# Kernel optimization log

Hardware: AMD Instinct MI355X
Metric: run time of the kernel (lower is better)

Reference implementation:

```python
import jax, jax.numpy as jnp
import numpy as np

B, N, C = 8, 2048, 3
E, H, NB, K = 256, 8, 3, 32
OUT_PTS = N // 2
EPS = 1e-5


def _ln(x, g, b):
    mu = jnp.mean(x, -1, keepdims=True)
    v = jnp.var(x, -1, keepdims=True)
    return g * (x - mu) / jnp.sqrt(v + EPS) + b


def _bn(x, g, b, axes):
    # train-mode BatchNorm1d: per-feature batch stats (biased variance)
    mu = jnp.mean(x, axes, keepdims=True)
    v = jnp.var(x, axes, keepdims=True)
    return g * (x - mu) / jnp.sqrt(v + EPS) + b


def setup_inputs() -> dict:
    key = jax.random.key(0)
    ks = jax.random.split(key, 20)
    rn = lambda k, shape, s: jax.random.normal(k, shape, jnp.float32) * s
    inp = {}
    inp['x'] = jax.random.normal(ks[0], (B, N, C), jnp.float32)
    # ARPE params
    inp['W1'] = rn(ks[1], (2 * C, 2 * C), 0.3)
    inp['b1'] = jnp.zeros((2 * C,), jnp.float32)
    inp['g1'] = jnp.ones((2 * C,), jnp.float32)
    inp['be1'] = jnp.zeros((2 * C,), jnp.float32)
    inp['W2'] = rn(ks[2], (2 * C, E), 0.3)
    inp['b2'] = jnp.zeros((E,), jnp.float32)
    inp['g2'] = jnp.ones((E,), jnp.float32)
    inp['be2'] = jnp.zeros((E,), jnp.float32)
    # transformer block params (stacked over NB blocks)
    inp['ln1_g'] = jnp.ones((NB, E), jnp.float32)
    inp['ln1_b'] = jnp.zeros((NB, E), jnp.float32)
    inp['attn_w'] = rn(ks[3], (NB, E, 3 * E), 0.02)
    inp['attn_b'] = jnp.zeros((NB, 3 * E), jnp.float32)
    inp['out_w'] = rn(ks[4], (NB, E, E), 0.02)
    inp['out_b'] = jnp.zeros((NB, E), jnp.float32)
    inp['ln2_g'] = jnp.ones((NB, E), jnp.float32)
    inp['ln2_b'] = jnp.zeros((NB, E), jnp.float32)
    inp['ff1_w'] = rn(ks[5], (NB, E, 2 * E), 0.02)
    inp['ff1_b'] = jnp.zeros((NB, 2 * E), jnp.float32)
    inp['ff2_w'] = rn(ks[6], (NB, 2 * E, E), 0.02)
    inp['ff2_b'] = jnp.zeros((NB, E), jnp.float32)
    # decoder params
    inp['dec1_w'] = rn(ks[7], (E, 2 * E), 0.02)
    inp['dec1_b'] = jnp.zeros((2 * E,), jnp.float32)
    inp['dec2_w'] = rn(ks[8], (2 * E, OUT_PTS * 3), 0.02)
    inp['dec2_b'] = jnp.zeros((OUT_PTS * 3,), jnp.float32)
    return inp


def _forward(x, W1, b1, g1, be1, W2, b2, g2, be2,
             ln1_g, ln1_b, attn_w, attn_b, out_w, out_b,
             ln2_g, ln2_b, ff1_w, ff1_b, ff2_w, ff2_b,
             dec1_w, dec1_b, dec2_w, dec2_b):
    Bv, Nv, Cv = x.shape
    # --- ARPE: KNN gather + diff-concat + MLP/BN/ELU + max-pool ---
    sq = jnp.sum(x * x, -1)  # [B,N]
    d2 = sq[:, :, None] + sq[:, None, :] - 2.0 * jnp.einsum('bnc,bmc->bnm', x, x)
    idx = jax.lax.top_k(-d2, K)[1]  # [B,N,K] nearest (incl. self)
    knn = jax.vmap(lambda pts, i: pts[i])(x, idx)  # [B,N,K,C]
    diffs = x[:, :, None, :] - knn
    feat = jnp.concatenate([jnp.broadcast_to(x[:, :, None, :], diffs.shape), diffs], -1)  # [B,N,K,2C]
    h = feat @ W1 + b1
    h = jax.nn.elu(_bn(h, g1, be1, (0, 1, 2)))
    h = jnp.max(h, axis=2)  # max-pool over K -> [B,N,2C]
    h = h @ W2 + b2
    h = jax.nn.elu(_bn(h, g2, be2, (0, 1)))  # [B,N,E]
    # --- transformer blocks (pre-LN; residual adds the LN'd x, per source) ---
    dh = E // H
    scale = 1.0 / np.sqrt(dh)
    xcur = h
    for i in range(NB):
        hn = _ln(xcur, ln1_g[i], ln1_b[i])
        qkv = hn @ attn_w[i] + attn_b[i]
        q, k_, v = jnp.split(qkv, 3, axis=-1)
        q = q.reshape(Bv, Nv, H, dh)
        k_ = k_.reshape(Bv, Nv, H, dh)
        v = v.reshape(Bv, Nv, H, dh)
        att = jax.nn.softmax(jnp.einsum('bnhd,bmhd->bhnm', q, k_) * scale, axis=-1)
        o = jnp.einsum('bhnm,bmhd->bnhd', att, v).reshape(Bv, Nv, E)
        xcur = o @ out_w[i] + out_b[i] + hn
        hn2 = _ln(xcur, ln2_g[i], ln2_b[i])
        ff = jax.nn.gelu(hn2 @ ff1_w[i] + ff1_b[i], approximate=False) @ ff2_w[i] + ff2_b[i]
        xcur = ff + xcur
    # --- decoder ---
    m = jnp.mean(xcur, axis=1)  # [B,E]
    d = jax.nn.gelu(m @ dec1_w + dec1_b, approximate=False) @ dec2_w + dec2_b
    return d.reshape(Bv, OUT_PTS, 3)


def reference(x, W1, b1, g1, be1, W2, b2, g2, be2,
              ln1_g, ln1_b, attn_w, attn_b, out_w, out_b,
              ln2_g, ln2_b, ff1_w, ff1_b, ff2_w, ff2_b,
              dec1_w, dec1_b, dec2_w, dec2_b):
    return _forward(x, W1, b1, g1, be1, W2, b2, g2, be2,
                    ln1_g, ln1_b, attn_w, attn_b, out_w, out_b,
                    ln2_g, ln2_b, ff1_w, ff1_b, ff2_w, ff2_b,
                    dec1_w, dec1_b, dec2_w, dec2_b)
```

## Files before the change

kernel.cpp:

```cpp
#include <hip/hip_runtime.h>
#include <math.h>
#include <float.h>

#define Bb 8
#define Nn 2048
#define Ee 256
#define Hh 8
#define NB 3
#define KK 32
#define DH 32
#define QKV 768
#define FF 512
#define OUTPTS 1024

#define CEXP 0.25509667991878083f

typedef __bf16 bf16x8 __attribute__((ext_vector_type(8)));
typedef __bf16 bf16x4 __attribute__((ext_vector_type(4)));
typedef float f32x4 __attribute__((ext_vector_type(4)));
typedef float f32x16 __attribute__((ext_vector_type(16)));
typedef unsigned u32x2 __attribute__((ext_vector_type(2)));

#if __has_builtin(__builtin_amdgcn_exp2f)
#define EXP2(x) __builtin_amdgcn_exp2f(x)
#else
#define EXP2(x) exp2f(x)
#endif

static __device__ __forceinline__ float geluf(float v) {
    return 0.5f * v * (1.0f + erff(v * 0.70710678118654752f));
}
static __device__ __forceinline__ float eluf(float v) {
    return v > 0.0f ? v : expm1f(v);
}
static __device__ __forceinline__ unsigned pkbf(float a, float b) {
    union { __bf16 h[2]; unsigned u; } t;
    t.h[0] = (__bf16)a; t.h[1] = (__bf16)b;
    return t.u;
}
static __device__ __forceinline__ void swap32(unsigned a, unsigned b, unsigned& outA, unsigned& outB, int hi) {
#if __has_builtin(__builtin_amdgcn_permlane32_swap)
    u32x2 r = __builtin_amdgcn_permlane32_swap(a, b, false, false);
    outA = r[0]; outB = r[1];
#else
    unsigned ax = (unsigned)__shfl_xor((int)a, 32, 64);
    unsigned bx = (unsigned)__shfl_xor((int)b, 32, 64);
    outB = hi ? ax : b;
    outA = hi ? a : bx;
#endif
}

#if __has_builtin(__builtin_amdgcn_global_load_lds)
#define HAVE_GLOAD_LDS 1
static __device__ __forceinline__ void gl_lds16(const __bf16* g, __bf16* l) {
    __builtin_amdgcn_global_load_lds(
        (const __attribute__((address_space(1))) unsigned*)g,
        (__attribute__((address_space(3))) unsigned*)l, 16, 0, 0);
}
#else
#define HAVE_GLOAD_LDS 0
#endif

__global__ __launch_bounds__(256) void k_knn(const float* __restrict__ x,
                                             int* __restrict__ idx) {
    int q = blockIdx.x * 4 + (threadIdx.x >> 6);
    int lane = threadIdx.x & 63;
    int b = q >> 11, n = q & (Nn - 1);
    const float* xb = x + (size_t)b * Nn * 3;
    float xn0 = xb[n * 3], xn1 = xb[n * 3 + 1], xn2 = xb[n * 3 + 2];
    float sqn = xn0 * xn0 + xn1 * xn1 + xn2 * xn2;

    unsigned cand[32];
#pragma unroll
    for (int c = 0; c < 32; ++c) {
        int m = lane + 64 * c;
        float xm0 = xb[m * 3], xm1 = xb[m * 3 + 1], xm2 = xb[m * 3 + 2];
        float sqm = xm0 * xm0 + xm1 * xm1 + xm2 * xm2;
        float d = sqn + sqm - 2.0f * (xn0 * xm0 + xn1 * xm1 + xn2 * xm2);
        unsigned fb = __float_as_uint(d);
        cand[c] = (fb & 0x80000000u) ? ~fb : (fb | 0x80000000u);
    }

    unsigned prefix = 0u;
    for (int bit = 31; bit >= 0; --bit) {
        unsigned t = prefix | (1u << bit);
        int cnt = 0;
#pragma unroll
        for (int c = 0; c < 32; ++c)
            cnt += (int)__popcll(__ballot(cand[c] < t));
        if (cnt < KK) prefix = t;
    }

    unsigned long long lmask = (1ULL << lane) - 1ULL;
    int base = 0;
#pragma unroll
    for (int c = 0; c < 32; ++c) {
        bool sel = cand[c] < prefix;
        unsigned long long mk = __ballot(sel);
        int pos = base + (int)__popcll(mk & lmask);
        if (sel) idx[(size_t)q * KK + pos] = lane + 64 * c;
        base += (int)__popcll(mk);
    }
    for (int c = 0; c < 32 && base < KK; ++c) {
        bool eq = (cand[c] == prefix);
        unsigned long long mk = __ballot(eq);
        int pos = base + (int)__popcll(mk & lmask);
        if (eq && pos < KK) idx[(size_t)q * KK + pos] = lane + 64 * c;
        base += (int)__popcll(mk);
    }
}

__global__ __launch_bounds__(256) void k_h1(const float* __restrict__ x, const int* __restrict__ idx,
                                            const float* __restrict__ W1, const float* __restrict__ b1,
                                            float* __restrict__ h1) {
    int t = blockIdx.x * 256 + threadIdx.x;
    if (t >= Bb * Nn * KK) return;
    int bn = t / KK;
    int b = bn / Nn, n = bn % Nn;
    int j = idx[t];
    const float* xb = x + (size_t)b * Nn * 3;
    float xn0 = xb[n * 3], xn1 = xb[n * 3 + 1], xn2 = xb[n * 3 + 2];
    float f3 = xn0 - xb[j * 3], f4 = xn1 - xb[j * 3 + 1], f5 = xn2 - xb[j * 3 + 2];
    float* o = h1 + (size_t)t * 6;
#pragma unroll
    for (int c = 0; c < 6; ++c) {
        o[c] = b1[c] + xn0 * W1[0 * 6 + c] + xn1 * W1[1 * 6 + c] + xn2 * W1[2 * 6 + c]
             + f3 * W1[3 * 6 + c] + f4 * W1[4 * 6 + c] + f5 * W1[5 * 6 + c];
    }
}

__global__ __launch_bounds__(256) void k_stats6_part(const float* __restrict__ v, int R, int nblk,
                                                     double* __restrict__ part) {
    int blk = blockIdx.x, tid = threadIdx.x;
    int rows = R / nblk;
    int r0 = blk * rows;
    double s[6] = {0, 0, 0, 0, 0, 0}, s2[6] = {0, 0, 0, 0, 0, 0};
    for (int r = r0 + tid; r < r0 + rows; r += 256) {
        const float* p = v + (size_t)r * 6;
#pragma unroll
        for (int c = 0; c < 6; ++c) { double t = p[c]; s[c] += t; s2[c] += t * t; }
    }
    __shared__ double sh[256][12];
#pragma unroll
    for (int c = 0; c < 6; ++c) { sh[tid][c] = s[c]; sh[tid][6 + c] = s2[c]; }
    __syncthreads();
    for (int st = 128; st > 0; st >>= 1) {
        if (tid < st) {
#pragma unroll
            for (int q = 0; q < 12; ++q) sh[tid][q] += sh[tid + st][q];
        }
        __syncthreads();
    }
    if (tid < 12) part[(size_t)blk * 12 + tid] = sh[0][tid];
}

__global__ __launch_bounds__(64) void k_stats6_fin(const double* __restrict__ part, int nblk, int R,
                                                   float* __restrict__ mean, float* __restrict__ rstd) {
    int q = threadIdx.x;
    __shared__ double tot[12];
    if (q < 12) {
        double s = 0.0;
        for (int b = 0; b < nblk; ++b) s += part[(size_t)b * 12 + q];
        tot[q] = s;
    }
    __syncthreads();
    if (q < 6) {
        double mu = tot[q] / R;
        double var = tot[6 + q] / R - mu * mu;
        mean[q] = (float)mu;
        rstd[q] = (float)(1.0 / sqrt(var + 1e-5));
    }
}

__global__ __launch_bounds__(256) void k_stats256_part(const float* __restrict__ v, int R, int nblk,
                                                       double* __restrict__ part) {
    int blk = blockIdx.x, c = threadIdx.x;
    int rows = R / nblk;
    int r0 = blk * rows;
    double s = 0.0, s2 = 0.0;
    for (int r = r0; r < r0 + rows; ++r) {
        double t = v[(size_t)r * Ee + c];
        s += t; s2 += t * t;
    }
    part[(size_t)blk * (2 * Ee) + c] = s;
    part[(size_t)blk * (2 * Ee) + Ee + c] = s2;
}

__global__ __launch_bounds__(256) void k_stats256_fin(const double* __restrict__ part, int nblk, int R,
                                                      float* __restrict__ mean, float* __restrict__ rstd) {
    int c = threadIdx.x;
    double s = 0.0, s2 = 0.0;
    for (int b = 0; b < nblk; ++b) {
        s += part[(size_t)b * (2 * Ee) + c];
        s2 += part[(size_t)b * (2 * Ee) + Ee + c];
    }
    double mu = s / R;
    double var = s2 / R - mu * mu;
    mean[c] = (float)mu;
    rstd[c] = (float)(1.0 / sqrt(var + 1e-5));
}

__global__ __launch_bounds__(256) void k_maxh2(const float* __restrict__ h1,
                                               const float* __restrict__ mean1, const float* __restrict__ rstd1,
                                               const float* __restrict__ g1, const float* __restrict__ be1,
                                               const float* __restrict__ W2, const float* __restrict__ b2,
                                               float* __restrict__ x0) {
    int bn = blockIdx.x;
    int t = threadIdx.x;
    __shared__ float hval[KK][6];
    __shared__ float hmax[6];
    if (t < KK * 6) {
        int k = t / 6, c = t % 6;
        float v = h1[((size_t)bn * KK + k) * 6 + c];
        v = (v - mean1[c]) * rstd1[c] * g1[c] + be1[c];
        hval[k][c] = eluf(v);
    }
    __syncthreads();
    if (t < 6) {
        float m = -FLT_MAX;
        for (int k = 0; k < KK; ++k) m = fmaxf(m, hval[k][t]);
        hmax[t] = m;
    }
    __syncthreads();
    float s = b2[t];
#pragma unroll
    for (int i = 0; i < 6; ++i) s += hmax[i] * W2[i * Ee + t];
    x0[(size_t)bn * Ee + t] = s;
}

__global__ __launch_bounds__(256) void k_bn2apply(float* __restrict__ x0,
                                                  const float* __restrict__ mean2, const float* __restrict__ rstd2,
                                                  const float* __restrict__ g2, const float* __restrict__ be2) {
    int i = blockIdx.x * 256 + threadIdx.x;
    if (i < Bb * Nn * Ee) {
        int c = i & (Ee - 1);
        float v = (x0[i] - mean2[c]) * rstd2[c] * g2[c] + be2[c];
        x0[i] = eluf(v);
    }
}

__global__ __launch_bounds__(256) void k_lnb(const float* __restrict__ X,
                                             const float* __restrict__ g, const float* __restrict__ b,
                                             __bf16* __restrict__ Yb) {
    int row = blockIdx.x * 4 + (threadIdx.x >> 6);
    int lane = threadIdx.x & 63;
    float4 v = *(const float4*)(X + (size_t)row * Ee + lane * 4);
    float s = v.x + v.y + v.z + v.w;
#pragma unroll
    for (int off = 32; off; off >>= 1) s += __shfl_xor(s, off, 64);
    float mu = s * (1.0f / Ee);
    float d0 = v.x - mu, d1 = v.y - mu, d2 = v.z - mu, d3 = v.w - mu;
    float s2 = d0 * d0 + d1 * d1 + d2 * d2 + d3 * d3;
#pragma unroll
    for (int off = 32; off; off >>= 1) s2 += __shfl_xor(s2, off, 64);
    float rstd = 1.0f / sqrtf(s2 * (1.0f / Ee) + 1e-5f);
    float4 gv = *(const float4*)(g + lane * 4);
    float4 bv = *(const float4*)(b + lane * 4);
    bf16x4 o;
    o[0] = (__bf16)(gv.x * d0 * rstd + bv.x);
    o[1] = (__bf16)(gv.y * d1 * rstd + bv.y);
    o[2] = (__bf16)(gv.z * d2 * rstd + bv.z);
    o[3] = (__bf16)(gv.w * d3 * rstd + bv.w);
    *(bf16x4*)(Yb + (size_t)row * Ee + lane * 4) = o;
}

__global__ __launch_bounds__(256) void k_wt(const float* __restrict__ w, __bf16* __restrict__ wt,
                                            int K, int N) {
    w += (size_t)blockIdx.z * K * N;
    wt += (size_t)blockIdx.z * K * N;
    int n0 = blockIdx.x * 64, k0 = blockIdx.y * 64;
    __shared__ float L[64][65];
    int t = threadIdx.x;
    int r = t >> 4, c4 = (t & 15) * 4;
#pragma unroll
    for (int j = 0; j < 4; ++j) {
        float4 v = *(const float4*)(w + (size_t)(k0 + r + j * 16) * N + n0 + c4);
        L[r + j * 16][c4 + 0] = v.x; L[r + j * 16][c4 + 1] = v.y;
        L[r + j * 16][c4 + 2] = v.z; L[r + j * 16][c4 + 3] = v.w;
    }
    __syncthreads();
#pragma unroll
    for (int j = 0; j < 4; ++j) {
        int nn = r + j * 16;
        bf16x4 o;
        o[0] = (__bf16)L[c4 + 0][nn]; o[1] = (__bf16)L[c4 + 1][nn];
        o[2] = (__bf16)L[c4 + 2][nn]; o[3] = (__bf16)L[c4 + 3][nn];
        *(bf16x4*)(wt + (size_t)(n0 + nn) * K + k0 + c4) = o;
    }
}

template<int OUTM, int RESM, int ACT, int QKVM>
__global__ __launch_bounds__(256) void k_mgemm(const __bf16* __restrict__ Ain,
                                               const __bf16* __restrict__ Wt,
                                               const float* __restrict__ bias,
                                               const void* __restrict__ res,
                                               void* __restrict__ out,
                                               int Kd, int Nd) {
    __shared__ __bf16 As[128 * 32];
    __shared__ __bf16 Bs[128 * 32];
    int tid = threadIdx.x;
    int n0 = blockIdx.x * 128, m0 = blockIdx.y * 128;
    int wave = tid >> 6, lane = tid & 63;
    int wr = wave >> 1, wc = wave & 1;
    int t = lane & 15, gg = lane >> 4;
    f32x4 acc[4][4];
#pragma unroll
    for (int m = 0; m < 4; ++m)
#pragma unroll
        for (int nn = 0; nn < 4; ++nn) acc[m][nn] = (f32x4){0.f, 0.f, 0.f, 0.f};
    int r0 = tid >> 2, g0 = tid & 3;
    int r1 = (tid + 256) >> 2, g1 = tid & 3;
    for (int kt = 0; kt < Kd; kt += 32) {
#if HAVE_GLOAD_LDS
        __syncthreads();
        gl_lds16(Ain + (size_t)(m0 + r0) * Kd + kt + g0 * 8, &As[r0 * 32 + g0 * 8]);
        gl_lds16(Ain + (size_t)(m0 + r1) * Kd + kt + g1 * 8, &As[r1 * 32 + g1 * 8]);
        gl_lds16(Wt + (size_t)(n0 + r0) * Kd + kt + g0 * 8, &Bs[r0 * 32 + g0 * 8]);
        gl_lds16(Wt + (size_t)(n0 + r1) * Kd + kt + g1 * 8, &Bs[r1 * 32 + g1 * 8]);
        __syncthreads();
#else
        bf16x8 a0 = *(const bf16x8*)(Ain + (size_t)(m0 + r0) * Kd + kt + g0 * 8);
        bf16x8 a1 = *(const bf16x8*)(Ain + (size_t)(m0 + r1) * Kd + kt + g1 * 8);
        bf16x8 w0 = *(const bf16x8*)(Wt + (size_t)(n0 + r0) * Kd + kt + g0 * 8);
        bf16x8 w1 = *(const bf16x8*)(Wt + (size_t)(n0 + r1) * Kd + kt + g1 * 8);
        __syncthreads();
        *(bf16x8*)&As[r0 * 32 + g0 * 8] = a0;
        *(bf16x8*)&As[r1 * 32 + g1 * 8] = a1;
        *(bf16x8*)&Bs[r0 * 32 + g0 * 8] = w0;
        *(bf16x8*)&Bs[r1 * 32 + g1 * 8] = w1;
        __syncthreads();
#endif
        bf16x8 af[4], bfr[4];
#pragma unroll
        for (int m = 0; m < 4; ++m) af[m] = *(const bf16x8*)&As[(wr * 64 + m * 16 + t) * 32 + gg * 8];
#pragma unroll
        for (int nn = 0; nn < 4; ++nn) bfr[nn] = *(const bf16x8*)&Bs[(wc * 64 + nn * 16 + t) * 32 + gg * 8];
#pragma unroll
        for (int m = 0; m < 4; ++m)
#pragma unroll
            for (int nn = 0; nn < 4; ++nn)
                acc[m][nn] = __builtin_amdgcn_mfma_f32_16x16x32_bf16(af[m], bfr[nn], acc[m][nn], 0, 0, 0);
    }
#pragma unroll
    for (int m = 0; m < 4; ++m) {
#pragma unroll
        for (int nn = 0; nn < 4; ++nn) {
            int ocol = n0 + wc * 64 + nn * 16 + t;
            float bv = bias[ocol];
#pragma unroll
            for (int j = 0; j < 4; ++j) {
                int orow = m0 + wr * 64 + m * 16 + gg * 4 + j;
                float v = acc[m][nn][j] + bv;
                if (RESM == 1) v += (float)((const __bf16*)res)[(size_t)orow * Nd + ocol];
                if (RESM == 2) v += ((const float*)res)[(size_t)orow * Nd + ocol];
                if (ACT == 1) v = geluf(v);
                if (QKVM == 1 && ocol < Ee) v *= CEXP;
                if (OUTM == 0) ((float*)out)[(size_t)orow * Nd + ocol] = v;
                else           ((__bf16*)out)[(size_t)orow * Nd + ocol] = (__bf16)v;
            }
        }
    }
}

__global__ __launch_bounds__(256) void k_attn(const __bf16* __restrict__ qkv, __bf16* __restrict__ obf) {
    int wgid = (blockIdx.x & 7) * 128 + (blockIdx.x >> 3);
    int qg = wgid & 15;
    int bh = wgid >> 4;
    int h = bh & 7, b = bh >> 3;
    int wave = threadIdx.x >> 6, lane = threadIdx.x & 63;
    int l31 = lane & 31, hi = lane >> 5;
    int qb = qg * 128 + wave * 32;
    const size_t base = (size_t)b * Nn * QKV;

    const __bf16* qrow = qkv + base + (size_t)(qb + l31) * QKV + h * DH;
    bf16x8 qf0 = *(const bf16x8*)(qrow + hi * 8);
    bf16x8 qf1 = *(const bf16x8*)(qrow + 16 + hi * 8);

    const __bf16* vbase = qkv + base + 2 * Ee + h * DH + l31;

    f32x16 oacc = {0.f,0.f,0.f,0.f,0.f,0.f,0.f,0.f,0.f,0.f,0.f,0.f,0.f,0.f,0.f,0.f};
    float lsum = 0.0f;

    for (int c0 = 0; c0 < Nn; c0 += 32) {
        const __bf16* krow = qkv + base + (size_t)(c0 + l31) * QKV + Ee + h * DH;
        bf16x8 kf0 = *(const bf16x8*)(krow + hi * 8);
        bf16x8 kf1 = *(const bf16x8*)(krow + 16 + hi * 8);

        f32x16 s = {0.f,0.f,0.f,0.f,0.f,0.f,0.f,0.f,0.f,0.f,0.f,0.f,0.f,0.f,0.f,0.f};
        s = __builtin_amdgcn_mfma_f32_32x32x16_bf16(kf0, qf0, s, 0, 0, 0);
        s = __builtin_amdgcn_mfma_f32_32x32x16_bf16(kf1, qf1, s, 0, 0, 0);

        float p[16];
#pragma unroll
        for (int i = 0; i < 16; ++i) p[i] = EXP2(s[i]);
        float s0 = (p[0] + p[1]) + (p[2] + p[3]);
        float s1 = (p[4] + p[5]) + (p[6] + p[7]);
        float s2r = (p[8] + p[9]) + (p[10] + p[11]);
        float s3 = (p[12] + p[13]) + (p[14] + p[15]);
        lsum += (s0 + s1) + (s2r + s3);

        unsigned d0 = pkbf(p[0], p[1]),  d1 = pkbf(p[2], p[3]);
        unsigned d2 = pkbf(p[4], p[5]),  d3 = pkbf(p[6], p[7]);
        unsigned d4 = pkbf(p[8], p[9]),  d5 = pkbf(p[10], p[11]);
        unsigned d6 = pkbf(p[12], p[13]), d7 = pkbf(p[14], p[15]);
        unsigned w0a, w0b, w1a, w1b, w2a, w2b, w3a, w3b;
        swap32(d2, d0, w2a, w0a, hi);
        swap32(d3, d1, w3a, w1a, hi);
        swap32(d6, d4, w2b, w0b, hi);
        swap32(d7, d5, w3b, w1b, hi);
        union { unsigned u[4]; bf16x8 v; } pa0, pa1;
        pa0.u[0] = w0a; pa0.u[1] = w1a; pa0.u[2] = w2a; pa0.u[3] = w3a;
        pa1.u[0] = w0b; pa1.u[1] = w1b; pa1.u[2] = w2b; pa1.u[3] = w3b;

        union { __bf16 hh[8]; bf16x8 v; } vf0, vf1;
        const __bf16* vp = vbase + (size_t)(c0 + hi * 8) * QKV;
#pragma unroll
        for (int j = 0; j < 8; ++j) vf0.hh[j] = vp[(size_t)j * QKV];
#pragma unroll
        for (int j = 0; j < 8; ++j) vf1.hh[j] = vp[(size_t)(16 + j) * QKV];

        oacc = __builtin_amdgcn_mfma_f32_32x32x16_bf16(pa0.v, vf0.v, oacc, 0, 0, 0);
        oacc = __builtin_amdgcn_mfma_f32_32x32x16_bf16(pa1.v, vf1.v, oacc, 0, 0, 0);
    }

    float ltot = lsum + __shfl_xor(lsum, 32, 64);
    float invl = 1.0f / ltot;
#pragma unroll
    for (int reg = 0; reg < 16; ++reg) {
        int row = (reg & 3) + 8 * (reg >> 2) + 4 * hi;
        float iv = __shfl(invl, row, 64);
        obf[((size_t)(b * Nn + qb + row)) * Ee + h * DH + l31] = (__bf16)(oacc[reg] * iv);
    }
}

__global__ __launch_bounds__(256) void k_meanpart(const float* __restrict__ X, float* __restrict__ pm) {
    int chunk = blockIdx.x, b = blockIdx.y;
    int e = threadIdx.x;
    float s = 0.0f;
    for (int n = chunk * 256; n < chunk * 256 + 256; ++n)
        s += X[((size_t)b * Nn + n) * Ee + e];
    pm[(size_t)(b * 8 + chunk) * Ee + e] = s;
}
__global__ __launch_bounds__(256) void k_meanfin(const float* __restrict__ pm, float* __restrict__ m) {
    int i = blockIdx.x * 256 + threadIdx.x;
    int b = i >> 8, e = i & 255;
    float s = 0.0f;
    for (int c = 0; c < 8; ++c) s += pm[(size_t)(b * 8 + c) * Ee + e];
    m[i] = s * (1.0f / Nn);
}
__global__ __launch_bounds__(512) void k_dec1(const float* __restrict__ m, const float* __restrict__ w,
                                              const float* __restrict__ bias, float* __restrict__ t1) {
    int b = blockIdx.x, j = threadIdx.x;
    float s = bias[j];
    for (int i = 0; i < Ee; ++i) s += m[b * Ee + i] * w[i * FF + j];
    t1[b * FF + j] = geluf(s);
}
__global__ __launch_bounds__(256) void k_dec2(const float* __restrict__ t1, const float* __restrict__ w,
                                              const float* __restrict__ bias, float* __restrict__ out) {
    int i = blockIdx.x * 256 + threadIdx.x;
    int b = i / 3072, j = i % 3072;
    float s = bias[j];
    for (int k = 0; k < FF; ++k) s += t1[b * FF + k] * w[k * 3072 + j];
    out[i] = s;
}

extern "C" void kernel_launch(void* const* d_in, const int* in_sizes, int n_in,
                              void* d_out, int out_size, void* d_ws, size_t ws_size,
                              hipStream_t stream) {
    const float* x      = (const float*)d_in[0];
    const float* W1     = (const float*)d_in[1];
    const float* b1     = (const float*)d_in[2];
    const float* g1     = (const float*)d_in[3];
    const float* be1    = (const float*)d_in[4];
    const float* W2     = (const float*)d_in[5];
    const float* b2     = (const float*)d_in[6];
    const float* g2     = (const float*)d_in[7];
    const float* be2    = (const float*)d_in[8];
    const float* ln1_g  = (const float*)d_in[9];
    const float* ln1_b  = (const float*)d_in[10];
    const float* attn_w = (const float*)d_in[11];
    const float* attn_b = (const float*)d_in[12];
    const float* out_w  = (const float*)d_in[13];
    const float* out_b  = (const float*)d_in[14];
    const float* ln2_g  = (const float*)d_in[15];
    const float* ln2_b  = (const float*)d_in[16];
    const float* ff1_w  = (const float*)d_in[17];
    const float* ff1_b  = (const float*)d_in[18];
    const float* ff2_w  = (const float*)d_in[19];
    const float* ff2_b  = (const float*)d_in[20];
    const float* dec1_w = (const float*)d_in[21];
    const float* dec1_b = (const float*)d_in[22];
    const float* dec2_w = (const float*)d_in[23];
    const float* dec2_b = (const float*)d_in[24];
    (void)in_sizes; (void)n_in; (void)out_size; (void)ws_size;

    const size_t MN = (size_t)Bb * Nn * Ee;

    float*  A    = (float*)d_ws;
    __bf16* Ab   = (__bf16*)(A + MN);
    __bf16* qkvb = Ab + MN;
    __bf16* obf  = qkvb + (size_t)Bb * Nn * QKV;
    __bf16* ffb  = obf + MN;
    __bf16* attn_wt = ffb + (size_t)Bb * Nn * FF;
    __bf16* out_wt  = attn_wt + (size_t)NB * QKV * Ee;
    __bf16* ff1_wt  = out_wt + (size_t)NB * Ee * Ee;
    __bf16* ff2_wt  = ff1_wt + (size_t)NB * FF * Ee;
    float*  S       = (float*)(ff2_wt + (size_t)NB * Ee * FF);

    float* mean1 = S,      *rstd1 = S + 16;
    float* mean2 = S + 32, *rstd2 = S + 32 + Ee;
    float* pm    = S + 1024;
    float* mvec  = pm + 64 * Ee;
    float* t1    = mvec + Bb * Ee;
    double* part6   = (double*)(S + 32768);
    double* part256 = part6 + 512 * 12;

    int*   idx = (int*)qkvb;
    float* h1  = (float*)(idx + (size_t)Bb * Nn * KK);

    k_wt<<<dim3(QKV / 64, Ee / 64, NB), 256, 0, stream>>>(attn_w, attn_wt, Ee, QKV);
    k_wt<<<dim3(Ee / 64, Ee / 64, NB), 256, 0, stream>>>(out_w, out_wt, Ee, Ee);
    k_wt<<<dim3(FF / 64, Ee / 64, NB), 256, 0, stream>>>(ff1_w, ff1_wt, Ee, FF);
    k_wt<<<dim3(Ee / 64, FF / 64, NB), 256, 0, stream>>>(ff2_w, ff2_wt, FF, Ee);

    k_knn <<<Bb * Nn / 4, 256, 0, stream>>>(x, idx);
    k_h1  <<<(Bb * Nn * KK) / 256, 256, 0, stream>>>(x, idx, W1, b1, h1);
    k_stats6_part<<<512, 256, 0, stream>>>(h1, Bb * Nn * KK, 512, part6);
    k_stats6_fin<<<1, 64, 0, stream>>>(part6, 512, Bb * Nn * KK, mean1, rstd1);
    k_maxh2<<<Bb * Nn, 256, 0, stream>>>(h1, mean1, rstd1, g1, be1, W2, b2, A);
    k_stats256_part<<<64, 256, 0, stream>>>(A, Bb * Nn, 64, part256);
    k_stats256_fin<<<1, 256, 0, stream>>>(part256, 64, Bb * Nn, mean2, rstd2);
    k_bn2apply<<<(Bb * Nn * Ee) / 256, 256, 0, stream>>>(A, mean2, rstd2, g2, be2);

    const int M = Bb * Nn;
    for (int i = 0; i < NB; ++i) {
        k_lnb<<<M / 4, 256, 0, stream>>>(A, ln1_g + i * Ee, ln1_b + i * Ee, Ab);
        k_mgemm<1, 0, 0, 1><<<dim3(QKV / 128, M / 128), 256, 0, stream>>>(
            Ab, attn_wt + (size_t)i * QKV * Ee, attn_b + i * QKV, nullptr, qkvb, Ee, QKV);
        k_attn<<<Bb * Hh * 16, 256, 0, stream>>>(qkvb, obf);
        k_mgemm<0, 1, 0, 0><<<dim3(Ee / 128, M / 128), 256, 0, stream>>>(
            obf, out_wt + (size_t)i * Ee * Ee, out_b + i * Ee, Ab, A, Ee, Ee);
        k_lnb<<<M / 4, 256, 0, stream>>>(A, ln2_g + i * Ee, ln2_b + i * Ee, Ab);
        k_mgemm<1, 0, 1, 0><<<dim3(FF / 128, M / 128), 256, 0, stream>>>(
            Ab, ff1_wt + (size_t)i * FF * Ee, ff1_b + i * FF, nullptr, ffb, Ee, FF);
        k_mgemm<0, 2, 0, 0><<<dim3(Ee / 128, M / 128), 256, 0, stream>>>(
            ffb, ff2_wt + (size_t)i * Ee * FF, ff2_b + i * Ee, A, A, FF, Ee);
    }

    k_meanpart<<<dim3(8, Bb), 256, 0, stream>>>(A, pm);
    k_meanfin<<<Bb, 256, 0, stream>>>(pm, mvec);
    k_dec1<<<Bb, FF, 0, stream>>>(mvec, dec1_w, dec1_b, t1);
    k_dec2<<<(Bb * OUTPTS * 3) / 256, 256, 0, stream>>>(t1, dec2_w, dec2_b, (float*)d_out);
}
```

Baseline: 887.1 us.

## Software-pipeline K/V loads in attention and merge weight-transpose launches

The attention inner loop now processes two 32-key chunks per iteration. The next chunk's K and V fragments are prefetched into registers while the current chunk runs its MFMAs, and two separate output accumulators shorten the MFMA dependency chain. This is meant to hide global load latency in the attention kernel, at the cost of more registers and possibly lower occupancy. Separately, the four weight-transpose launches are folded into one kernel that dispatches on block index, removing three launches.

```diff
diff --git a/kernel.cpp b/kernel.cpp
--- a/kernel.cpp
+++ b/kernel.cpp
@@ -264,11 +264,29 @@
     *(bf16x4*)(Yb + (size_t)row * Ee + lane * 4) = o;
 }
 
-__global__ __launch_bounds__(256) void k_wt(const float* __restrict__ w, __bf16* __restrict__ wt,
-                                            int K, int N) {
-    w += (size_t)blockIdx.z * K * N;
-    wt += (size_t)blockIdx.z * K * N;
-    int n0 = blockIdx.x * 64, k0 = blockIdx.y * 64;
+__global__ __launch_bounds__(256) void k_wtall(const float* __restrict__ attn_w, const float* __restrict__ out_w,
+                                               const float* __restrict__ ff1_w, const float* __restrict__ ff2_w,
+                                               __bf16* __restrict__ attn_wt, __bf16* __restrict__ out_wt,
+                                               __bf16* __restrict__ ff1_wt, __bf16* __restrict__ ff2_wt) {
+    int bid = blockIdx.x;
+    const float* w; __bf16* wt; int K, N, n0, k0;
+    if (bid < 144) {
+        int r = bid; int z = r / 48; r %= 48;
+        K = Ee; N = QKV; n0 = (r % 12) * 64; k0 = (r / 12) * 64;
+        w = attn_w + (size_t)z * K * N; wt = attn_wt + (size_t)z * K * N;
+    } else if (bid < 192) {
+        int r = bid - 144; int z = r / 16; r %= 16;
+        K = Ee; N = Ee; n0 = (r % 4) * 64; k0 = (r / 4) * 64;
+        w = out_w + (size_t)z * K * N; wt = out_wt + (size_t)z * K * N;
+    } else if (bid < 288) {
+        int r = bid - 192; int z = r / 32; r %= 32;
+        K = Ee; N = FF; n0 = (r % 8) * 64; k0 = (r / 8) * 64;
+        w = ff1_w + (size_t)z * K * N; wt = ff1_wt + (size_t)z * K * N;
+    } else {
+        int r = bid - 288; int z = r / 32; r %= 32;
+        K = FF; N = Ee; n0 = (r % 4) * 64; k0 = (r / 4) * 64;
+        w = ff2_w + (size_t)z * K * N; wt = ff2_wt + (size_t)z * K * N;
+    }
     __shared__ float L[64][65];
     int t = threadIdx.x;
     int r = t >> 4, c4 = (t & 15) * 4;
@@ -376,20 +394,31 @@
     bf16x8 qf0 = *(const bf16x8*)(qrow + hi * 8);
     bf16x8 qf1 = *(const bf16x8*)(qrow + 16 + hi * 8);
 
+    const __bf16* kbase = qkv + base + Ee + h * DH + (size_t)l31 * QKV;
     const __bf16* vbase = qkv + base + 2 * Ee + h * DH + l31;
 
-    f32x16 oacc = {0.f,0.f,0.f,0.f,0.f,0.f,0.f,0.f,0.f,0.f,0.f,0.f,0.f,0.f,0.f,0.f};
+    f32x16 oaccA = {0.f,0.f,0.f,0.f,0.f,0.f,0.f,0.f,0.f,0.f,0.f,0.f,0.f,0.f,0.f,0.f};
+    f32x16 oaccB = oaccA;
     float lsum = 0.0f;
 
-    for (int c0 = 0; c0 < Nn; c0 += 32) {
-        const __bf16* krow = qkv + base + (size_t)(c0 + l31) * QKV + Ee + h * DH;
-        bf16x8 kf0 = *(const bf16x8*)(krow + hi * 8);
-        bf16x8 kf1 = *(const bf16x8*)(krow + 16 + hi * 8);
-
+    auto loadK = [&](int c, bf16x8& k0, bf16x8& k1) {
+        const __bf16* kr = kbase + (size_t)c * QKV;
+        k0 = *(const bf16x8*)(kr + hi * 8);
+        k1 = *(const bf16x8*)(kr + 16 + hi * 8);
+    };
+    auto loadV = [&](int c, bf16x8& v0, bf16x8& v1) {
+        union { __bf16 hh[8]; bf16x8 v; } a, bb;
+        const __bf16* vp = vbase + (size_t)(c + hi * 8) * QKV;
+#pragma unroll
+        for (int j = 0; j < 8; ++j) a.hh[j] = vp[(size_t)j * QKV];
+#pragma unroll
+        for (int j = 0; j < 8; ++j) bb.hh[j] = vp[(size_t)(16 + j) * QKV];
+        v0 = a.v; v1 = bb.v;
+    };
+    auto compute = [&](bf16x8 k0, bf16x8 k1, bf16x8 v0, bf16x8 v1, f32x16& oacc) {
         f32x16 s = {0.f,0.f,0.f,0.f,0.f,0.f,0.f,0.f,0.f,0.f,0.f,0.f,0.f,0.f,0.f,0.f};
-        s = __builtin_amdgcn_mfma_f32_32x32x16_bf16(kf0, qf0, s, 0, 0, 0);
-        s = __builtin_amdgcn_mfma_f32_32x32x16_bf16(kf1, qf1, s, 0, 0, 0);
-
+        s = __builtin_amdgcn_mfma_f32_32x32x16_bf16(k0, qf0, s, 0, 0, 0);
+        s = __builtin_amdgcn_mfma_f32_32x32x16_bf16(k1, qf1, s, 0, 0, 0);
         float p[16];
 #pragma unroll
         for (int i = 0; i < 16; ++i) p[i] = EXP2(s[i]);
@@ -412,16 +441,21 @@
         pa0.u[0] = w0a; pa0.u[1] = w1a; pa0.u[2] = w2a; pa0.u[3] = w3a;
         pa1.u[0] = w0b; pa1.u[1] = w1b; pa1.u[2] = w2b; pa1.u[3] = w3b;
 
-        union { __bf16 hh[8]; bf16x8 v; } vf0, vf1;
-        const __bf16* vp = vbase + (size_t)(c0 + hi * 8) * QKV;
-#pragma unroll
-        for (int j = 0; j < 8; ++j) vf0.hh[j] = vp[(size_t)j * QKV];
-#pragma unroll
-        for (int j = 0; j < 8; ++j) vf1.hh[j] = vp[(size_t)(16 + j) * QKV];
-
-        oacc = __builtin_amdgcn_mfma_f32_32x32x16_bf16(pa0.v, vf0.v, oacc, 0, 0, 0);
-        oacc = __builtin_amdgcn_mfma_f32_32x32x16_bf16(pa1.v, vf1.v, oacc, 0, 0, 0);
-    }
+        oacc = __builtin_amdgcn_mfma_f32_32x32x16_bf16(pa0.v, v0, oacc, 0, 0, 0);
+        oacc = __builtin_amdgcn_mfma_f32_32x32x16_bf16(pa1.v, v1, oacc, 0, 0, 0);
+    };
+
+    bf16x8 k0a, k1a, v0a, v1a, k0b, k1b, v0b, v1b;
+    loadK(0, k0a, k1a); loadV(0, v0a, v1a);
+    for (int c0 = 0; c0 < Nn; c0 += 64) {
+        loadK(c0 + 32, k0b, k1b); loadV(c0 + 32, v0b, v1b);
+        compute(k0a, k1a, v0a, v1a, oaccA);
+        if (c0 + 64 < Nn) {
+            loadK(c0 + 64, k0a, k1a); loadV(c0 + 64, v0a, v1a);
+        }
+        compute(k0b, k1b, v0b, v1b, oaccB);
+    }
+    f32x16 oacc = oaccA + oaccB;
 
     float ltot = lsum + __shfl_xor(lsum, 32, 64);
     float invl = 1.0f / ltot;
@@ -518,10 +552,8 @@
     int*   idx = (int*)qkvb;
     float* h1  = (float*)(idx + (size_t)Bb * Nn * KK);
 
-    k_wt<<<dim3(QKV / 64, Ee / 64, NB), 256, 0, stream>>>(attn_w, attn_wt, Ee, QKV);
-    k_wt<<<dim3(Ee / 64, Ee / 64, NB), 256, 0, stream>>>(out_w, out_wt, Ee, Ee);
-    k_wt<<<dim3(FF / 64, Ee / 64, NB), 256, 0, stream>>>(ff1_w, ff1_wt, Ee, FF);
-    k_wt<<<dim3(Ee / 64, FF / 64, NB), 256, 0, stream>>>(ff2_w, ff2_wt, FF, Ee);
+    k_wtall<<<384, 256, 0, stream>>>(attn_w, out_w, ff1_w, ff2_w,
+                                     attn_wt, out_wt, ff1_wt, ff2_wt);
 
     k_knn <<<Bb * Nn / 4, 256, 0, stream>>>(x, idx);
     k_h1  <<<(Bb * Nn * KK) / 256, 256, 0, stream>>>(x, idx, W1, b1, h1);
```

After: 951.1 us. 1.07x slower.

## Split attention over key halves with merge kernel; fuse weight transposes

Applied to the files above, without the earlier changes.

Attention now splits the key range in two, doubling the grid, and writes unnormalized partial outputs and row sums. A new merge kernel adds the two partials and divides by the combined sum. The four weight-transpose launches are merged into one kernel that dispatches on block index. This adds extra global traffic for the partial outputs and one more launch per block, in exchange for more parallelism in attention.

```diff
diff --git a/kernel.cpp b/kernel.cpp
--- a/kernel.cpp
+++ b/kernel.cpp
@@ -264,11 +264,29 @@
     *(bf16x4*)(Yb + (size_t)row * Ee + lane * 4) = o;
 }
 
-__global__ __launch_bounds__(256) void k_wt(const float* __restrict__ w, __bf16* __restrict__ wt,
-                                            int K, int N) {
-    w += (size_t)blockIdx.z * K * N;
-    wt += (size_t)blockIdx.z * K * N;
-    int n0 = blockIdx.x * 64, k0 = blockIdx.y * 64;
+__global__ __launch_bounds__(256) void k_wtall(const float* __restrict__ attn_w, const float* __restrict__ out_w,
+                                               const float* __restrict__ ff1_w, const float* __restrict__ ff2_w,
+                                               __bf16* __restrict__ attn_wt, __bf16* __restrict__ out_wt,
+                                               __bf16* __restrict__ ff1_wt, __bf16* __restrict__ ff2_wt) {
+    int bid = blockIdx.x;
+    const float* w; __bf16* wt; int K, N, n0, k0;
+    if (bid < 144) {
+        int r = bid; int z = r / 48; r %= 48;
+        K = Ee; N = QKV; n0 = (r % 12) * 64; k0 = (r / 12) * 64;
+        w = attn_w + (size_t)z * K * N; wt = attn_wt + (size_t)z * K * N;
+    } else if (bid < 192) {
+        int r = bid - 144; int z = r / 16; r %= 16;
+        K = Ee; N = Ee; n0 = (r % 4) * 64; k0 = (r / 4) * 64;
+        w = out_w + (size_t)z * K * N; wt = out_wt + (size_t)z * K * N;
+    } else if (bid < 288) {
+        int r = bid - 192; int z = r / 32; r %= 32;
+        K = Ee; N = FF; n0 = (r % 8) * 64; k0 = (r / 8) * 64;
+        w = ff1_w + (size_t)z * K * N; wt = ff1_wt + (size_t)z * K * N;
+    } else {
+        int r = bid - 288; int z = r / 32; r %= 32;
+        K = FF; N = Ee; n0 = (r % 4) * 64; k0 = (r / 4) * 64;
+        w = ff2_w + (size_t)z * K * N; wt = ff2_wt + (size_t)z * K * N;
+    }
     __shared__ float L[64][65];
     int t = threadIdx.x;
     int r = t >> 4, c4 = (t & 15) * 4;
@@ -362,15 +380,18 @@
     }
 }
 
-__global__ __launch_bounds__(256) void k_attn(const __bf16* __restrict__ qkv, __bf16* __restrict__ obf) {
-    int wgid = (blockIdx.x & 7) * 128 + (blockIdx.x >> 3);
+__global__ __launch_bounds__(256) void k_attn(const __bf16* __restrict__ qkv,
+                                              __bf16* __restrict__ pO, float* __restrict__ pl) {
+    int wgid = (blockIdx.x & 7) * 256 + (blockIdx.x >> 3);
     int qg = wgid & 15;
-    int bh = wgid >> 4;
+    int sk = (wgid >> 4) & 1;
+    int bh = wgid >> 5;
     int h = bh & 7, b = bh >> 3;
     int wave = threadIdx.x >> 6, lane = threadIdx.x & 63;
     int l31 = lane & 31, hi = lane >> 5;
     int qb = qg * 128 + wave * 32;
     const size_t base = (size_t)b * Nn * QKV;
+    const size_t MNc = (size_t)Bb * Nn * Ee;
 
     const __bf16* qrow = qkv + base + (size_t)(qb + l31) * QKV + h * DH;
     bf16x8 qf0 = *(const bf16x8*)(qrow + hi * 8);
@@ -381,7 +402,8 @@
     f32x16 oacc = {0.f,0.f,0.f,0.f,0.f,0.f,0.f,0.f,0.f,0.f,0.f,0.f,0.f,0.f,0.f,0.f};
     float lsum = 0.0f;
 
-    for (int c0 = 0; c0 < Nn; c0 += 32) {
+    int cbeg = sk * (Nn / 2);
+    for (int c0 = cbeg; c0 < cbeg + Nn / 2; c0 += 32) {
         const __bf16* krow = qkv + base + (size_t)(c0 + l31) * QKV + Ee + h * DH;
         bf16x8 kf0 = *(const bf16x8*)(krow + hi * 8);
         bf16x8 kf1 = *(const bf16x8*)(krow + 16 + hi * 8);
@@ -424,13 +446,25 @@
     }
 
     float ltot = lsum + __shfl_xor(lsum, 32, 64);
-    float invl = 1.0f / ltot;
+    if (hi == 0)
+        pl[(sk << 17) + (size_t)(b * Nn + qb + l31) * Hh + h] = ltot;
 #pragma unroll
     for (int reg = 0; reg < 16; ++reg) {
         int row = (reg & 3) + 8 * (reg >> 2) + 4 * hi;
-        float iv = __shfl(invl, row, 64);
-        obf[((size_t)(b * Nn + qb + row)) * Ee + h * DH + l31] = (__bf16)(oacc[reg] * iv);
-    }
+        pO[sk * MNc + ((size_t)(b * Nn + qb + row)) * Ee + h * DH + l31] = (__bf16)oacc[reg];
+    }
+}
+
+__global__ __launch_bounds__(256) void k_amerge(const __bf16* __restrict__ pO,
+                                                const float* __restrict__ pl,
+                                                __bf16* __restrict__ obf) {
+    const size_t MNc = (size_t)Bb * Nn * Ee;
+    int i = blockIdx.x * 256 + threadIdx.x;
+    int row = i >> 8;
+    int h = (i & 255) >> 5;
+    float l = pl[(size_t)row * Hh + h] + pl[(1 << 17) + (size_t)row * Hh + h];
+    float v = (float)pO[i] + (float)pO[MNc + i];
+    obf[i] = (__bf16)(v / l);
 }
 
 __global__ __launch_bounds__(256) void k_meanpart(const float* __restrict__ X, float* __restrict__ pm) {
@@ -514,14 +548,15 @@
     float* t1    = mvec + Bb * Ee;
     double* part6   = (double*)(S + 32768);
     double* part256 = part6 + 512 * 12;
+    float*  pl      = (float*)(part256 + 64 * 512);
+
+    __bf16* pO = ffb;
 
     int*   idx = (int*)qkvb;
     float* h1  = (float*)(idx + (size_t)Bb * Nn * KK);
 
-    k_wt<<<dim3(QKV / 64, Ee / 64, NB), 256, 0, stream>>>(attn_w, attn_wt, Ee, QKV);
-    k_wt<<<dim3(Ee / 64, Ee / 64, NB), 256, 0, stream>>>(out_w, out_wt, Ee, Ee);
-    k_wt<<<dim3(FF / 64, Ee / 64, NB), 256, 0, stream>>>(ff1_w, ff1_wt, Ee, FF);
-    k_wt<<<dim3(Ee / 64, FF / 64, NB), 256, 0, stream>>>(ff2_w, ff2_wt, FF, Ee);
+    k_wtall<<<384, 256, 0, stream>>>(attn_w, out_w, ff1_w, ff2_w,
+                                     attn_wt, out_wt, ff1_wt, ff2_wt);
 
     k_knn <<<Bb * Nn / 4, 256, 0, stream>>>(x, idx);
     k_h1  <<<(Bb * Nn * KK) / 256, 256, 0, stream>>>(x, idx, W1, b1, h1);
@@ -537,7 +572,8 @@
         k_lnb<<<M / 4, 256, 0, stream>>>(A, ln1_g + i * Ee, ln1_b + i * Ee, Ab);
         k_mgemm<1, 0, 0, 1><<<dim3(QKV / 128, M / 128), 256, 0, stream>>>(
             Ab, attn_wt + (size_t)i * QKV * Ee, attn_b + i * QKV, nullptr, qkvb, Ee, QKV);
-        k_attn<<<Bb * Hh * 16, 256, 0, stream>>>(qkvb, obf);
+        k_attn<<<2 * Bb * Hh * 16, 256, 0, stream>>>(qkvb, pO, pl);
+        k_amerge<<<MN / 256, 256, 0, stream>>>(pO, pl, obf);
         k_mgemm<0, 1, 0, 0><<<dim3(Ee / 128, M / 128), 256, 0, stream>>>(
             obf, out_wt + (size_t)i * Ee * Ee, out_b + i * Ee, Ab, A, Ee, Ee);
         k_lnb<<<M / 4, 256, 0, stream>>>(A, ln2_g + i * Ee, ln2_b + i * Ee, Ab);
```

Measured after the change: 908.9 us. +2.5%, slower.
